# Optimization experiments

Measured on AMD Instinct MI355X. Metric: run time of the kernel, lower is better.

## Reference

```python
import jax, jax.numpy as jnp
import numpy as np

FEAT = 256       # feat_size
GROUPS = 8       # num_groups for GroupNorm
EPS = 1e-5       # torch GroupNorm default eps
K_SAMPLES = 100  # inference_samples
LEVEL_LENS = [16384, 4096, 1024, 256]  # flattened fH*fW per pyramid level
BATCH = 8


def _group_norm(x, scale, bias):
    # x: [B, C, L]; normalize per (batch, group) over (C//G, L)
    B, C, L = x.shape
    xg = x.reshape(B, GROUPS, C // GROUPS, L)
    mu = xg.mean(axis=(2, 3), keepdims=True)
    var = xg.var(axis=(2, 3), keepdims=True)
    xn = ((xg - mu) * jax.lax.rsqrt(var + EPS)).reshape(B, C, L)
    return xn * scale[None, :, None] + bias[None, :, None]


def _head(x, gn1_scale, gn1_bias, W1, b1, gn2_scale, gn2_bias, W2, b2):
    # hidden block: GroupNorm -> ReLU -> Conv1d(k=1) == per-pixel matmul
    h = jax.nn.relu(_group_norm(x, gn1_scale, gn1_bias))
    h = jnp.einsum('oc,bcl->bol', W1, h) + b1[None, :, None]
    # final block: GroupNorm -> ReLU -> Conv1d(C -> 1, k=1)
    h = jax.nn.relu(_group_norm(h, gn2_scale, gn2_bias))
    return jnp.einsum('oc,bcl->bol', W2, h) + b2[None, :, None]  # [B, 1, L]


def setup_inputs() -> dict:
    key = jax.random.key(0)
    ks = jax.random.split(key, 12)
    inp = {}
    for i, L in enumerate(LEVEL_LENS):
        inp[f'x{i}'] = jax.random.normal(ks[i], (BATCH, FEAT, L), dtype=jnp.float32)
    inp['gn1_scale'] = 1.0 + 0.1 * jax.random.normal(ks[4], (FEAT,), dtype=jnp.float32)
    inp['gn1_bias'] = 0.1 * jax.random.normal(ks[5], (FEAT,), dtype=jnp.float32)
    inp['W1'] = jax.random.normal(ks[6], (FEAT, FEAT), dtype=jnp.float32) / np.sqrt(FEAT)
    inp['b1'] = 0.01 * jax.random.normal(ks[7], (FEAT,), dtype=jnp.float32)
    inp['gn2_scale'] = 1.0 + 0.1 * jax.random.normal(ks[8], (FEAT,), dtype=jnp.float32)
    inp['gn2_bias'] = 0.1 * jax.random.normal(ks[9], (FEAT,), dtype=jnp.float32)
    inp['W2'] = jax.random.normal(ks[10], (1, FEAT), dtype=jnp.float32) / np.sqrt(FEAT)
    inp['b2'] = 0.01 * jax.random.normal(ks[11], (1,), dtype=jnp.float32)
    return inp


def reference(x0, x1, x2, x3, gn1_scale, gn1_bias, W1, b1, gn2_scale, gn2_bias, W2, b2):
    # inference path of PolicyNet (input_type='pyramid', eval mode)
    params = (gn1_scale, gn1_bias, W1, b1, gn2_scale, gn2_bias, W2, b2)
    logit_maps = [_head(x, *params) for x in (x0, x1, x2, x3)]
    logits = jnp.concatenate([lm.reshape(lm.shape[0], -1) for lm in logit_maps], axis=1)  # [B, sum(L)]
    # argsort descending, keep top inference_samples
    sample_ids = jax.lax.top_k(logits, K_SAMPLES)[1]  # [B, K]
    return sample_ids, logits
```

## Files before the change

kernel.cpp:

```cpp
#include <hip/hip_runtime.h>
#include <hip/hip_bf16.h>


#define B_ 8
#define C_ 256
#define G_ 8
#define P_ 21760
#define EPSV 1e-5f
#define XSS 264
#define XHALF (64 * XSS)
#define XBUF (2 * XHALF)
#define NTILES 2720

typedef __attribute__((ext_vector_type(4))) float floatx4;
typedef __attribute__((ext_vector_type(8))) __bf16 bf16x8;

__device__ __constant__ int kL[4]   = {16384, 4096, 1024, 256};
__device__ __constant__ int kOFF[4] = {0, 16384, 20480, 21504};

__device__ __forceinline__ void bf16split(float v, ushort& hi, ushort& lo) {
    __hip_bfloat16 h = __float2bfloat16(v);
    float hf = __bfloat162float(h);
    __hip_bfloat16 l = __float2bfloat16(v - hf);
    hi = *reinterpret_cast<ushort*>(&h);
    lo = *reinterpret_cast<ushort*>(&l);
}

__device__ __forceinline__ unsigned fkey(float f) {
    unsigned u = __float_as_uint(f);
    if (u == 0x80000000u) u = 0u;
    return (u & 0x80000000u) ? ~u : (u | 0x80000000u);
}

__global__ __launch_bounds__(256) void k_stats1(const float* __restrict__ x0,
                                                const float* __restrict__ x1,
                                                const float* __restrict__ x2,
                                                const float* __restrict__ x3,
                                                const float* __restrict__ W1,
                                                ushort* __restrict__ Whi,
                                                ushort* __restrict__ Wlo,
                                                float* __restrict__ part1) {
    int chunk = blockIdx.x, b = blockIdx.y, t = threadIdx.x;
    int flat = b * 85 + chunk;
    if (flat < 256) {
        int i = flat * 256 + t;
        ushort h, l;
        bf16split(W1[i], h, l);
        Whi[i] = h; Wlo[i] = l;
    }
    int lvl = chunk < 64 ? 0 : (chunk < 80 ? 1 : (chunk < 84 ? 2 : 3));
    const float* xp = lvl == 0 ? x0 : lvl == 1 ? x1 : lvl == 2 ? x2 : x3;
    int Ll = kL[lvl];
    int w = t >> 6, lane = t & 63;
    int l = chunk * 256 - kOFF[lvl] + lane * 4;
    __shared__ float redS[32], redQ[32];
    for (int g = 0; g < 8; ++g) {
        float s = 0.f, q = 0.f;
#pragma unroll
        for (int it = 0; it < 8; ++it) {
            int c = g * 32 + w * 8 + it;
            floatx4 v = *reinterpret_cast<const floatx4*>(xp + (b * 256 + c) * Ll + l);
            s += v.x + v.y + v.z + v.w;
            q += v.x * v.x + v.y * v.y + v.z * v.z + v.w * v.w;
        }
        for (int off = 32; off; off >>= 1) {
            s += __shfl_xor(s, off, 64);
            q += __shfl_xor(q, off, 64);
        }
        if (lane == 0) { redS[g * 4 + w] = s; redQ[g * 4 + w] = q; }
    }
    __syncthreads();
    if (t < 8) {
        float S = redS[t * 4] + redS[t * 4 + 1] + redS[t * 4 + 2] + redS[t * 4 + 3];
        float Q = redQ[t * 4] + redQ[t * 4 + 1] + redQ[t * 4 + 2] + redQ[t * 4 + 3];
        part1[((b * 85 + chunk) * 8 + t) * 2]     = S;
        part1[((b * 85 + chunk) * 8 + t) * 2 + 1] = Q;
    }
}

__global__ __launch_bounds__(64) void k_finalize(const float* __restrict__ part, int div,
                                                 const float* __restrict__ gsc,
                                                 const float* __restrict__ gbi,
                                                 float* __restrict__ ab) {
    int blk = blockIdx.x;
    int b = blk >> 5, lvl = (blk >> 3) & 3, g = blk & 7;
    int lane = threadIdx.x;
    int start = kOFF[lvl] / div, cnt = kL[lvl] / div, nch = P_ / div;
    float s = 0.f, q = 0.f;
    for (int m = lane; m < cnt; m += 64) {
        const float* p = part + ((b * nch + start + m) * 8 + g) * 2;
        s += p[0]; q += p[1];
    }
    for (int off = 32; off; off >>= 1) {
        s += __shfl_xor(s, off, 64);
        q += __shfl_xor(q, off, 64);
    }
    float N = 32.f * (float)kL[lvl];
    float mean = s / N;
    float var = q / N - mean * mean;
    float inv = rsqrtf(var + EPSV);
    if (lane < 32) {
        int c = g * 32 + lane;
        float a = inv * gsc[c];
        ab[(b * 4 + lvl) * 256 + c] = a;
        ab[8192 + (b * 4 + lvl) * 256 + c] = gbi[c] - mean * a;
    }
}

template <int MODE>
__global__ __launch_bounds__(512) void k_gemm(
    const float* __restrict__ x0, const float* __restrict__ x1,
    const float* __restrict__ x2, const float* __restrict__ x3,
    const ushort* __restrict__ Whi, const ushort* __restrict__ Wlo,
    const float* __restrict__ ab1, const float* __restrict__ b1,
    float* __restrict__ part2, const float* __restrict__ ab2,
    const float* __restrict__ W2, const float* __restrict__ b2,
    float* __restrict__ outF) {
    __shared__ ushort Xs[2 * XBUF];
    __shared__ float sRed[32 * 64];

    int t = threadIdx.x;
    int wv = t >> 6, lane = t & 63, lr = lane & 15, kg = lane >> 4;
    int ob = wv * 32;
    int px = lane;
    int cb = wv * 32;

    bf16x8 awh[8][2], awl[8][2];
#pragma unroll
    for (int kk = 0; kk < 8; ++kk)
#pragma unroll
        for (int mi = 0; mi < 2; ++mi) {
            int o = ob + mi * 16 + lr;
            awh[kk][mi] = *reinterpret_cast<const bf16x8*>(Whi + o * 256 + kk * 32 + 8 * kg);
            awl[kk][mi] = *reinterpret_cast<const bf16x8*>(Wlo + o * 256 + kk * 32 + 8 * kg);
        }

    int tid0 = blockIdx.x;
    {
        int b = tid0 / 340, tile = tid0 % 340;
        int lvl = tile < 256 ? 0 : (tile < 320 ? 1 : (tile < 336 ? 2 : 3));
        const float* xp = lvl == 0 ? x0 : lvl == 1 ? x1 : lvl == 2 ? x2 : x3;
        const float* a1p  = ab1 + (b * 4 + lvl) * 256;
        const float* be1p = a1p + 8192;
        const float* xc = xp + (b * 256 + cb) * kL[lvl] + (tile * 64 - kOFF[lvl]) + px;
        int Ll = kL[lvl];
        float xv[32];
#pragma unroll
        for (int u = 0; u < 32; ++u) xv[u] = xc[u * Ll];
#pragma unroll
        for (int q8 = 0; q8 < 4; ++q8) {
            alignas(16) ushort hs[8], ls[8];
#pragma unroll
            for (int u = 0; u < 8; ++u) {
                int c = cb + q8 * 8 + u;
                bf16split(fmaxf(fmaf(a1p[c], xv[q8 * 8 + u], be1p[c]), 0.f), hs[u], ls[u]);
            }
            *reinterpret_cast<uint4*>(&Xs[px * XSS + cb + q8 * 8]) =
                *reinterpret_cast<const uint4*>(hs);
            *reinterpret_cast<uint4*>(&Xs[XHALF + px * XSS + cb + q8 * 8]) =
                *reinterpret_cast<const uint4*>(ls);
        }
    }

    int cur = 0;
    for (int tid = tid0; tid < NTILES; tid += 256) {
        int b = tid / 340, tile = tid % 340;
        int lvl = tile < 256 ? 0 : (tile < 320 ? 1 : (tile < 336 ? 2 : 3));

        int ntid = tid + 256;
        bool have = ntid < NTILES;
        float nxv[32];
        const float *na1p = nullptr, *nbe1p = nullptr;
        if (have) {
            int nb = ntid / 340, ntile = ntid % 340;
            int nlvl = ntile < 256 ? 0 : (ntile < 320 ? 1 : (ntile < 336 ? 2 : 3));
            const float* nxp = nlvl == 0 ? x0 : nlvl == 1 ? x1 : nlvl == 2 ? x2 : x3;
            na1p  = ab1 + (nb * 4 + nlvl) * 256;
            nbe1p = na1p + 8192;
            int nLl = kL[nlvl];
            const float* nxc = nxp + (nb * 256 + cb) * nLl + (ntile * 64 - kOFF[nlvl]) + px;
#pragma unroll
            for (int u = 0; u < 32; ++u) nxv[u] = nxc[u * nLl];
        }

        __syncthreads();

        const ushort* XH = Xs + cur * XBUF;
        const ushort* XL = XH + XHALF;

        floatx4 acc[2][4];
#pragma unroll
        for (int mi = 0; mi < 2; ++mi)
#pragma unroll
            for (int ni = 0; ni < 4; ++ni) acc[mi][ni] = (floatx4){0.f, 0.f, 0.f, 0.f};

#pragma unroll
        for (int kk = 0; kk < 8; ++kk) {
            bf16x8 bh[4], bl[4];
#pragma unroll
            for (int ni = 0; ni < 4; ++ni) {
                int p = ni * 16 + lr;
                bh[ni] = *reinterpret_cast<const bf16x8*>(&XH[p * XSS + kk * 32 + 8 * kg]);
                bl[ni] = *reinterpret_cast<const bf16x8*>(&XL[p * XSS + kk * 32 + 8 * kg]);
            }
#pragma unroll
            for (int mi = 0; mi < 2; ++mi)
#pragma unroll
                for (int ni = 0; ni < 4; ++ni) {
                    acc[mi][ni] = __builtin_amdgcn_mfma_f32_16x16x32_bf16(awh[kk][mi], bh[ni], acc[mi][ni], 0, 0, 0);
                    acc[mi][ni] = __builtin_amdgcn_mfma_f32_16x16x32_bf16(awh[kk][mi], bl[ni], acc[mi][ni], 0, 0, 0);
                    acc[mi][ni] = __builtin_amdgcn_mfma_f32_16x16x32_bf16(awl[kk][mi], bh[ni], acc[mi][ni], 0, 0, 0);
                }
        }

        floatx4 b1f[2];
#pragma unroll
        for (int mi = 0; mi < 2; ++mi)
            b1f[mi] = *reinterpret_cast<const floatx4*>(b1 + ob + mi * 16 + 4 * kg);
#pragma unroll
        for (int mi = 0; mi < 2; ++mi)
#pragma unroll
            for (int ni = 0; ni < 4; ++ni)
#pragma unroll
                for (int r = 0; r < 4; ++r)
                    acc[mi][ni][r] += b1f[mi][r];

        if (MODE == 0) {
            float s = 0.f, q = 0.f;
#pragma unroll
            for (int mi = 0; mi < 2; ++mi)
#pragma unroll
                for (int ni = 0; ni < 4; ++ni)
#pragma unroll
                    for (int r = 0; r < 4; ++r) {
                        float yv = acc[mi][ni][r];
                        s += yv; q += yv * yv;
                    }
            for (int off = 32; off; off >>= 1) {
                s += __shfl_xor(s, off, 64);
                q += __shfl_xor(q, off, 64);
            }
            if (lane == 0) {
                int base = (b * 340 + tile) * 8;
                part2[(base + wv) * 2]     = s;
                part2[(base + wv) * 2 + 1] = q;
            }
        } else {
            const float* a2p  = ab2 + (b * 4 + lvl) * 256;
            const float* be2p = a2p + 8192;
            float sj[4] = {0.f, 0.f, 0.f, 0.f};
#pragma unroll
            for (int mi = 0; mi < 2; ++mi) {
                int o4 = ob + mi * 16 + 4 * kg;
                floatx4 a2f  = *reinterpret_cast<const floatx4*>(a2p + o4);
                floatx4 be2f = *reinterpret_cast<const floatx4*>(be2p + o4);
                floatx4 w2f  = *reinterpret_cast<const floatx4*>(W2 + o4);
#pragma unroll
                for (int r = 0; r < 4; ++r) {
                    float a2 = a2f[r], be2 = be2f[r], w2 = w2f[r];
#pragma unroll
                    for (int ni = 0; ni < 4; ++ni) {
                        float h = fmaxf(fmaf(a2, acc[mi][ni][r], be2), 0.f);
                        sj[ni] = fmaf(w2, h, sj[ni]);
                    }
                }
            }
#pragma unroll
            for (int ni = 0; ni < 4; ++ni)
                sRed[(wv * 4 + kg) * 64 + ni * 16 + lr] = sj[ni];
            __syncthreads();
            if (t < 64) {
                float lg = b2[0];
#pragma unroll
                for (int m = 0; m < 32; ++m) lg += sRed[m * 64 + t];
                outF[800 + b * P_ + tile * 64 + t] = lg;
            }
        }

        if (have) {
            ushort* DH = Xs + (cur ^ 1) * XBUF;
            ushort* DL = DH + XHALF;
#pragma unroll
            for (int q8 = 0; q8 < 4; ++q8) {
                alignas(16) ushort hs[8], ls[8];
#pragma unroll
                for (int u = 0; u < 8; ++u) {
                    int c = cb + q8 * 8 + u;
                    bf16split(fmaxf(fmaf(na1p[c], nxv[q8 * 8 + u], nbe1p[c]), 0.f), hs[u], ls[u]);
                }
                *reinterpret_cast<uint4*>(&DH[px * XSS + cb + q8 * 8]) =
                    *reinterpret_cast<const uint4*>(hs);
                *reinterpret_cast<uint4*>(&DL[px * XSS + cb + q8 * 8]) =
                    *reinterpret_cast<const uint4*>(ls);
            }
        }
        cur ^= 1;
    }
}

__global__ __launch_bounds__(1024) void k_topk(const float* __restrict__ outF,
                                               float* __restrict__ outIds) {
    int b = blockIdx.x, t = threadIdx.x;
    int lane = t & 63;
    __shared__ unsigned hist[256];
    __shared__ unsigned scan[256];
    __shared__ unsigned wsum[4];
    __shared__ unsigned s_pref, s_K, s_iref, s_K2;
    __shared__ unsigned s_cnt;
    __shared__ unsigned long long cand[128];

    const float* src = outF + 800 + b * P_;
    unsigned key[22];
#pragma unroll
    for (int m = 0; m < 21; ++m) key[m] = fkey(src[t + m * 1024]);
    key[21] = (t < 256) ? fkey(src[t + 21504]) : 0u;
    bool has22 = (t < 256);

    if (t == 0) { s_K = 100; s_pref = 0; }

#pragma unroll
    for (int p = 0; p < 4; ++p) {
        int shift = 24 - 8 * p;
        for (int i = t; i < 256; i += 1024) hist[i] = 0;
        __syncthreads();
        unsigned pref = s_pref;
#pragma unroll
        for (int m = 0; m < 22; ++m) {
            if (m < 21 || has22) {
                unsigned u = key[m];
                if (p == 0 || (u >> (shift + 8)) == pref)
                    atomicAdd(&hist[(u >> shift) & 255], 1u);
            }
        }
        __syncthreads();
        unsigned inc = 0, hv = 0;
        if (t < 256) {
            hv = hist[t];
            inc = hv;
#pragma unroll
            for (int off = 1; off < 64; off <<= 1) {
                unsigned u = __shfl_up(inc, off, 64);
                if (lane >= off) inc += u;
            }
            if (lane == 63) wsum[t >> 6] = inc;
        }
        __syncthreads();
        if (t < 256) {
            unsigned base = 0;
#pragma unroll
            for (int w = 0; w < 4; ++w) if (w < (t >> 6)) base += wsum[w];
            unsigned P = base + inc;
            unsigned T4 = wsum[0] + wsum[1] + wsum[2] + wsum[3];
            scan[t] = T4 - P + hv;
        }
        __syncthreads();
        unsigned K = s_K;
        if (t < 256) {
            unsigned above = (t == 255) ? 0u : scan[t + 1];
            if (scan[t] >= K && above < K) {
                s_pref = (s_pref << 8) | (unsigned)t;
                s_K = K - above;
            }
        }
        __syncthreads();
    }
    unsigned T = s_pref;
    if (t == 0) { s_K2 = s_K; s_iref = 0; }
    __syncthreads();

#pragma unroll
    for (int p = 0; p < 2; ++p) {
        int shift = 8 - 8 * p;
        for (int i = t; i < 256; i += 1024) hist[i] = 0;
        __syncthreads();
        unsigned iref = s_iref;
#pragma unroll
        for (int m = 0; m < 22; ++m) {
            if (m < 21 || has22) {
                unsigned u = key[m];
                unsigned idx = (unsigned)(t + m * 1024);
                if (u == T && (p == 0 || (idx >> 8) == iref))
                    atomicAdd(&hist[(idx >> shift) & 255], 1u);
            }
        }
        __syncthreads();
        unsigned inc = 0;
        if (t < 256) {
            inc = hist[t];
#pragma unroll
            for (int off = 1; off < 64; off <<= 1) {
                unsigned u = __shfl_up(inc, off, 64);
                if (lane >= off) inc += u;
            }
            if (lane == 63) wsum[t >> 6] = inc;
        }
        __syncthreads();
        if (t < 256) {
            unsigned base = 0;
#pragma unroll
            for (int w = 0; w < 4; ++w) if (w < (t >> 6)) base += wsum[w];
            scan[t] = base + inc;
        }
        __syncthreads();
        unsigned K2 = s_K2;
        if (t < 256) {
            unsigned below = (t == 0) ? 0u : scan[t - 1];
            if (scan[t] >= K2 && below < K2) {
                s_iref = (s_iref << 8) | (unsigned)t;
                s_K2 = K2 - below;
            }
        }
        __syncthreads();
    }
    unsigned Ti = s_iref;

    if (t == 0) s_cnt = 0;
    if (t < 128) cand[t] = 0ull;
    __syncthreads();
#pragma unroll
    for (int m = 0; m < 22; ++m) {
        if (m < 21 || has22) {
            unsigned u = key[m];
            unsigned idx = (unsigned)(t + m * 1024);
            if (u > T || (u == T && idx <= Ti)) {
                unsigned p = atomicAdd(&s_cnt, 1u);
                if (p < 128)
                    cand[p] = ((unsigned long long)u << 32) | (unsigned long long)(0xFFFFFFFFu - idx);
            }
        }
    }
    __syncthreads();

    for (unsigned k = 2; k <= 128; k <<= 1) {
        for (unsigned j = k >> 1; j > 0; j >>= 1) {
            if (t < 128) {
                unsigned i = t, ixj = i ^ j;
                if (ixj > i) {
                    unsigned long long a = cand[i], c = cand[ixj];
                    bool desc = ((i & k) == 0);
                    if ((a < c) == desc) { cand[i] = c; cand[ixj] = a; }
                }
            }
            __syncthreads();
        }
    }
    if (t < 100) {
        unsigned idx = 0xFFFFFFFFu - (unsigned)(cand[t] & 0xFFFFFFFFull);
        outIds[b * 100 + t] = (float)idx;
    }
}

extern "C" void kernel_launch(void* const* d_in, const int* in_sizes, int n_in,
                              void* d_out, int out_size, void* d_ws, size_t ws_size,
                              hipStream_t stream) {
    const float* x0  = (const float*)d_in[0];
    const float* x1  = (const float*)d_in[1];
    const float* x2  = (const float*)d_in[2];
    const float* x3  = (const float*)d_in[3];
    const float* g1s = (const float*)d_in[4];
    const float* g1b = (const float*)d_in[5];
    const float* W1  = (const float*)d_in[6];
    const float* b1  = (const float*)d_in[7];
    const float* g2s = (const float*)d_in[8];
    const float* g2b = (const float*)d_in[9];
    const float* W2  = (const float*)d_in[10];
    const float* b2  = (const float*)d_in[11];
    float* outF = (float*)d_out;
    float* ws = (float*)d_ws;

    float*  ab1   = ws;
    float*  ab2   = ws + 16384;
    float*  U     = ws + 32768;
    float*  part1 = U;
    float*  part2 = U;
    ushort* Whi   = (ushort*)(ws + 76288);
    ushort* Wlo   = (ushort*)(ws + 109056);

    k_stats1<<<dim3(85, 8), dim3(256), 0, stream>>>(x0, x1, x2, x3, W1, Whi, Wlo, part1);
    k_finalize<<<dim3(256), dim3(64), 0, stream>>>(part1, 256, g1s, g1b, ab1);
    k_gemm<0><<<dim3(256), dim3(512), 0, stream>>>(x0, x1, x2, x3, Whi, Wlo, ab1, b1,
                                                   part2, ab2, W2, b2, outF);
    k_finalize<<<dim3(256), dim3(64), 0, stream>>>(part2, 64, g2s, g2b, ab2);
    k_gemm<2><<<dim3(256), dim3(512), 0, stream>>>(x0, x1, x2, x3, Whi, Wlo, ab1, b1,
                                                   part2, ab2, W2, b2, outF);
    k_topk<<<dim3(8), dim3(1024), 0, stream>>>(outF, outF);
}
```

Baseline: 199.5 us.

## Cache split-bf16 normalized activations for second GEMM pass instead of recomputing

The first GEMM pass now writes the GroupNorm+ReLU'd activations, already split into bf16 hi/lo pairs in an MFMA-ready layout, to a workspace buffer. A new kernel, k_gemm2, reads these directly from global memory with one block per tile and skips re-reading the fp32 input and re-normalizing. It trades the fp32 re-read plus split arithmetic for an extra write and read of a bf16 buffer about the same size as the input. It also loads W fragments from global per tile instead of holding them in registers, and only runs when the workspace is large enough.

After: 281.7 us. 41.2% more time.

```diff
diff --git a/kernel.cpp b/kernel.cpp
--- a/kernel.cpp
+++ b/kernel.cpp
@@ -115,7 +115,7 @@
     const float* __restrict__ ab1, const float* __restrict__ b1,
     float* __restrict__ part2, const float* __restrict__ ab2,
     const float* __restrict__ W2, const float* __restrict__ b2,
-    float* __restrict__ outF) {
+    ushort* __restrict__ Xbf, float* __restrict__ outF) {
     __shared__ ushort Xs[2 * XBUF];
     __shared__ float sRed[32 * 64];
 
@@ -159,6 +159,11 @@
                 *reinterpret_cast<const uint4*>(hs);
             *reinterpret_cast<uint4*>(&Xs[XHALF + px * XSS + cb + q8 * 8]) =
                 *reinterpret_cast<const uint4*>(ls);
+            if (MODE == 1) {
+                ushort* xb = Xbf + (size_t)tid0 * 32768 + ((wv * 4 + q8) * 64 + lane) * 8;
+                *reinterpret_cast<uint4*>(xb)         = *reinterpret_cast<const uint4*>(hs);
+                *reinterpret_cast<uint4*>(xb + 16384) = *reinterpret_cast<const uint4*>(ls);
+            }
         }
     }
 
@@ -225,7 +230,7 @@
                 for (int r = 0; r < 4; ++r)
                     acc[mi][ni][r] += b1f[mi][r];
 
-        if (MODE == 0) {
+        if (MODE == 0 || MODE == 1) {
             float s = 0.f, q = 0.f;
 #pragma unroll
             for (int mi = 0; mi < 2; ++mi)
@@ -292,9 +297,104 @@
                     *reinterpret_cast<const uint4*>(hs);
                 *reinterpret_cast<uint4*>(&DL[px * XSS + cb + q8 * 8]) =
                     *reinterpret_cast<const uint4*>(ls);
+                if (MODE == 1) {
+                    ushort* xb = Xbf + (size_t)ntid * 32768 + ((wv * 4 + q8) * 64 + lane) * 8;
+                    *reinterpret_cast<uint4*>(xb)         = *reinterpret_cast<const uint4*>(hs);
+                    *reinterpret_cast<uint4*>(xb + 16384) = *reinterpret_cast<const uint4*>(ls);
+                }
             }
         }
         cur ^= 1;
+    }
+}
+
+__global__ __launch_bounds__(512) void k_gemm2(
+    const ushort* __restrict__ Xbf,
+    const ushort* __restrict__ Whi, const ushort* __restrict__ Wlo,
+    const float* __restrict__ b1, const float* __restrict__ ab2,
+    const float* __restrict__ W2, const float* __restrict__ b2,
+    float* __restrict__ outF) {
+    __shared__ float sRed[32 * 64];
+    int tid = blockIdx.x;
+    int b = tid / 340, tile = tid % 340;
+    int t = threadIdx.x;
+    int wv = t >> 6, lane = t & 63, lr = lane & 15, kg = lane >> 4;
+    int ob = wv * 32;
+    int lvl = tile < 256 ? 0 : (tile < 320 ? 1 : (tile < 336 ? 2 : 3));
+    const ushort* xb = Xbf + (size_t)tid * 32768;
+
+    floatx4 acc[2][4];
+#pragma unroll
+    for (int mi = 0; mi < 2; ++mi)
+#pragma unroll
+        for (int ni = 0; ni < 4; ++ni) acc[mi][ni] = (floatx4){0.f, 0.f, 0.f, 0.f};
+
+#pragma unroll
+    for (int kk = 0; kk < 8; ++kk) {
+        bf16x8 ah[2], al[2], bh[4], bl[4];
+#pragma unroll
+        for (int mi = 0; mi < 2; ++mi) {
+            int o = ob + mi * 16 + lr;
+            ah[mi] = *reinterpret_cast<const bf16x8*>(Whi + o * 256 + kk * 32 + 8 * kg);
+            al[mi] = *reinterpret_cast<const bf16x8*>(Wlo + o * 256 + kk * 32 + 8 * kg);
+        }
+#pragma unroll
+        for (int ni = 0; ni < 4; ++ni) {
+            int p = ni * 16 + lr;
+            const ushort* q = xb + ((kk * 4 + kg) * 64 + p) * 8;
+            bh[ni] = *reinterpret_cast<const bf16x8*>(q);
+            bl[ni] = *reinterpret_cast<const bf16x8*>(q + 16384);
+        }
+#pragma unroll
+        for (int mi = 0; mi < 2; ++mi)
+#pragma unroll
+            for (int ni = 0; ni < 4; ++ni) {
+                acc[mi][ni] = __builtin_amdgcn_mfma_f32_16x16x32_bf16(ah[mi], bh[ni], acc[mi][ni], 0, 0, 0);
+                acc[mi][ni] = __builtin_amdgcn_mfma_f32_16x16x32_bf16(ah[mi], bl[ni], acc[mi][ni], 0, 0, 0);
+                acc[mi][ni] = __builtin_amdgcn_mfma_f32_16x16x32_bf16(al[mi], bh[ni], acc[mi][ni], 0, 0, 0);
+            }
+    }
+
+    floatx4 b1f[2];
+#pragma unroll
+    for (int mi = 0; mi < 2; ++mi)
+        b1f[mi] = *reinterpret_cast<const floatx4*>(b1 + ob + mi * 16 + 4 * kg);
+#pragma unroll
+    for (int mi = 0; mi < 2; ++mi)
+#pragma unroll
+        for (int ni = 0; ni < 4; ++ni)
+#pragma unroll
+            for (int r = 0; r < 4; ++r)
+                acc[mi][ni][r] += b1f[mi][r];
+
+    const float* a2p  = ab2 + (b * 4 + lvl) * 256;
+    const float* be2p = a2p + 8192;
+    float sj[4] = {0.f, 0.f, 0.f, 0.f};
+#pragma unroll
+    for (int mi = 0; mi < 2; ++mi) {
+        int o4 = ob + mi * 16 + 4 * kg;
+        floatx4 a2f  = *reinterpret_cast<const floatx4*>(a2p + o4);
+        floatx4 be2f = *reinterpret_cast<const floatx4*>(be2p + o4);
+        floatx4 w2f  = *reinterpret_cast<const floatx4*>(W2 + o4);
+#pragma unroll
+        for (int r = 0; r < 4; ++r) {
+            float a2 = a2f[r], be2 = be2f[r], w2 = w2f[r];
+#pragma unroll
+            for (int ni = 0; ni < 4; ++ni) {
+                float h = fmaxf(fmaf(a2, acc[mi][ni][r], be2), 0.f);
+                sj[ni] = fmaf(w2, h, sj[ni]);
+            }
+        }
+    }
+#pragma unroll
+    for (int ni = 0; ni < 4; ++ni)
+        sRed[(wv * 4 + kg) * 64 + ni * 16 + lr] = sj[ni];
+    __syncthreads();
+    if (t < 64) {
+        float lg = b2[0];
+#pragma unroll
+        for (int m = 0; m < 32; ++m) lg += sRed[m * 64 + t];
+        outF[800 + b * P_ + tile * 64 + t] = lg;
     }
 }
 
@@ -475,13 +575,22 @@
     float*  part2 = U;
     ushort* Whi   = (ushort*)(ws + 76288);
     ushort* Wlo   = (ushort*)(ws + 109056);
+    ushort* Xbf   = (ushort*)(ws + 141824);
+    bool useX = ws_size >= (size_t)(141824 + 44564480) * 4;
 
     k_stats1<<<dim3(85, 8), dim3(256), 0, stream>>>(x0, x1, x2, x3, W1, Whi, Wlo, part1);
     k_finalize<<<dim3(256), dim3(64), 0, stream>>>(part1, 256, g1s, g1b, ab1);
-    k_gemm<0><<<dim3(256), dim3(512), 0, stream>>>(x0, x1, x2, x3, Whi, Wlo, ab1, b1,
-                                                   part2, ab2, W2, b2, outF);
-    k_finalize<<<dim3(256), dim3(64), 0, stream>>>(part2, 64, g2s, g2b, ab2);
-    k_gemm<2><<<dim3(256), dim3(512), 0, stream>>>(x0, x1, x2, x3, Whi, Wlo, ab1, b1,
-                                                   part2, ab2, W2, b2, outF);
+    if (useX) {
+        k_gemm<1><<<dim3(256), dim3(512), 0, stream>>>(x0, x1, x2, x3, Whi, Wlo, ab1, b1,
+                                                       part2, ab2, W2, b2, Xbf, outF);
+        k_finalize<<<dim3(256), dim3(64), 0, stream>>>(part2, 64, g2s, g2b, ab2);
+        k_gemm2<<<dim3(NTILES), dim3(512), 0, stream>>>(Xbf, Whi, Wlo, b1, ab2, W2, b2, outF);
+    } else {
+        k_gemm<0><<<dim3(256), dim3(512), 0, stream>>>(x0, x1, x2, x3, Whi, Wlo, ab1, b1,
+                                                       part2, ab2, W2, b2, Xbf, outF);
+        k_finalize<<<dim3(256), dim3(64), 0, stream>>>(part2, 64, g2s, g2b, ab2);
+        k_gemm<2><<<dim3(256), dim3(512), 0, stream>>>(x0, x1, x2, x3, Whi, Wlo, ab1, b1,
+                                                       part2, ab2, W2, b2, Xbf, outF);
+    }
     k_topk<<<dim3(8), dim3(1024), 0, stream>>>(outF, outF);
 }
```
